# Optimization experiments

Hardware: AMD Instinct MI355X
Metric: run time of the kernel (lower is better)

## Reference

```python
import jax, jax.numpy as jnp
import numpy as np

TEMP = 1.0
EPS = 1e-3  # keras LayerNormalization default epsilon


def _ln(x, g, b):
    m = jnp.mean(x, -1, keepdims=True)
    v = jnp.mean((x - m) ** 2, -1, keepdims=True)
    return g * (x - m) * jax.lax.rsqrt(v + EPS) + b


def setup_inputs() -> dict:
    key = jax.random.key(0)
    ks = jax.random.split(key, 16)
    B, N, C, A, F = 8, 2048, 64, 256, 128
    r = lambda k, s: (jax.random.normal(ks[k], s) * 0.02).astype(jnp.float32)
    z = lambda n: jnp.zeros((n,), jnp.float32)
    return {
        'spatial': jax.random.normal(ks[0], (B, N, C), jnp.float32),
        'frequency': jax.random.normal(ks[1], (B, N, C), jnp.float32),
        'wavelet': jax.random.normal(ks[2], (B, N, C), jnp.float32),
        'Ws': r(3, (C, A)), 'bs': z(A),
        'Wf': r(4, (C, A)), 'bf': z(A),
        'Ww': r(5, (C, A)), 'bw': z(A),
        'g1': jnp.ones((A,), jnp.float32), 'b1': z(A),
        'Wk': r(6, (A, F)), 'bk': z(F),
        'Wq': r(7, (A, F)), 'bq': z(F),
        'Wt': r(8, (A, F)), 'bt': z(F),
        'Wg': r(9, (F + 3, F)), 'bg': z(F),
        'Wfu': r(10, (3 * F, F)), 'bfu': z(F),
        'Wdf': r(11, (F, F)), 'bdf': z(F),
        'g2': jnp.ones((F,), jnp.float32), 'b2': z(F),
    }


def _forward(spatial, frequency, wavelet, Ws, bs, Wf, bf, Ww, bw, g1, b1,
             Wk, bk, Wq, bq, Wt, bt, Wg, bg, Wfu, bfu, Wdf, bdf, g2, b2):
    B = spatial.shape[0]
    # FeatureAlignment: per-domain Dense + shared LayerNorm
    aligned = [
        _ln(spatial @ Ws + bs, g1, b1),
        _ln(frequency @ Wf + bf, g1, b1),
        _ln(wavelet @ Ww + bw, g1, b1),
    ]  # each [B, N, A]
    # DomainCorrelation
    K = [a @ Wk + bk for a in aligned]  # [B, N, F]
    Q = [a @ Wq + bq for a in aligned]
    corr = jnp.zeros((B, 3, 3), spatial.dtype)
    for i in range(3):
        for j in range(i, 3):
            # queries from domain j, keys from domain i (as in original)
            s = jax.nn.softmax(jnp.einsum('bnd,bmd->bnm', Q[j], K[i]) / TEMP, axis=-1)
            m = jnp.mean(s, axis=(1, 2))  # [B]
            corr = corr.at[:, i, j].set(m)
            if i != j:
                corr = corr.at[:, j, i].set(m)
    # NOTE: original applies softmax over the batch axis of the [B] row means
    dw = [jax.nn.softmax(jnp.mean(corr[:, i, :], axis=1)) for i in range(3)]  # each [B]
    # FeatureTransfer
    corr_mean = jnp.mean(corr, axis=1)  # [B, 3]
    enhanced = []
    for a, w in zip(aligned, dw):
        t = a @ Wt + bt  # [B, N, F]
        N = t.shape[1]
        gin = jnp.concatenate([t, jnp.broadcast_to(corr_mean[:, None, :], (B, N, 3))], axis=-1)
        gate = jax.nn.sigmoid(gin @ Wg + bg)
        enhanced.append(t * gate * w[:, None, None])
    fused = jnp.concatenate(enhanced, axis=-1) @ Wfu + bfu  # [B, N, F]
    out = _ln(fused @ Wdf + bdf, g2, b2)
    return out, corr, dw, enhanced


def reference(spatial, frequency, wavelet, Ws, bs, Wf, bf, Ww, bw, g1, b1,
              Wk, bk, Wq, bq, Wt, bt, Wg, bg, Wfu, bfu, Wdf, bdf, g2, b2):
    out, corr, dw, enh = _forward(spatial, frequency, wavelet, Ws, bs, Wf, bf, Ww, bw,
                                  g1, b1, Wk, bk, Wq, bq, Wt, bt, Wg, bg, Wfu, bfu,
                                  Wdf, bdf, g2, b2)
    return (out, corr, dw[0], dw[1], dw[2], enh[0], enh[1], enh[2])
```

## Files before the change

### kernel.cpp

```cpp
#include <hip/hip_runtime.h>
#include <math.h>


typedef __attribute__((ext_vector_type(8))) short short8;
typedef __attribute__((ext_vector_type(4))) float f32x4;
#define MFMA(a, b, c) __builtin_amdgcn_mfma_f32_16x16x32_bf16(a, b, c, 0, 0, 0)

#define NTOK 32

#define WD0_B 0u
#define WD1_B 32768u
#define WD2_B 65536u
#define WT_B  98304u
#define WG_B  163840u
#define WF0_B 196608u
#define WF1_B 229376u
#define WF2_B 262144u
#define WDF_B 294912u

__device__ __forceinline__ unsigned short bf16rtn(float v) {
    unsigned u = __float_as_uint(v);
    unsigned r = u + 0x7FFFu + ((u >> 16) & 1u);
    return (unsigned short)(r >> 16);
}
__device__ __forceinline__ void split2(float v, unsigned short& h, unsigned short& l) {
    h = bf16rtn(v);
    float hf = __uint_as_float(((unsigned)h) << 16);
    l = bf16rtn(v - hf);
}
__device__ __forceinline__ float bf2f(unsigned short h) {
    return __uint_as_float(((unsigned)h) << 16);
}

__global__ __launch_bounds__(256) void prep_kernel(
    const float* __restrict__ Ws, const float* __restrict__ Wf,
    const float* __restrict__ Ww, const float* __restrict__ Wt,
    const float* __restrict__ Wg, const float* __restrict__ Wfu,
    const float* __restrict__ Wdf, unsigned short* __restrict__ ws)
{
    int s = blockIdx.x * 256 + threadIdx.x;
    const float* src; int K, N; unsigned base, S; int fi;
    if (s < 2048)      { src = Ws;            K = 64;  N = 256; base = WD0_B; S = 16384; fi = s; }
    else if (s < 4096) { src = Wf;            K = 64;  N = 256; base = WD1_B; S = 16384; fi = s - 2048; }
    else if (s < 6144) { src = Ww;            K = 64;  N = 256; base = WD2_B; S = 16384; fi = s - 4096; }
    else if (s < 10240){ src = Wt;            K = 256; N = 128; base = WT_B;  S = 32768; fi = s - 6144; }
    else if (s < 12288){ src = Wg;            K = 128; N = 128; base = WG_B;  S = 16384; fi = s - 10240; }
    else if (s < 14336){ src = Wfu;           K = 128; N = 128; base = WF0_B; S = 16384; fi = s - 12288; }
    else if (s < 16384){ src = Wfu + 16384;   K = 128; N = 128; base = WF1_B; S = 16384; fi = s - 14336; }
    else if (s < 18432){ src = Wfu + 32768;   K = 128; N = 128; base = WF2_B; S = 16384; fi = s - 16384; }
    else               { src = Wdf;           K = 128; N = 128; base = WDF_B; S = 16384; fi = s - 18432; }
    const int lane = fi & 63, frag = fi >> 6;
    const int KC = K >> 5;
    const int nt = frag / KC, kc = frag - nt * KC;
    const int n  = nt * 16 + (lane & 15);
    const int k0 = kc * 32 + (lane >> 4) * 8;
    short8 hv, lv;
    #pragma unroll
    for (int j = 0; j < 8; ++j) {
        unsigned short h, l;
        split2(src[(k0 + j) * N + n], h, l);
        hv[j] = (short)h; lv[j] = (short)l;
    }
    *(short8*)&ws[base + (unsigned)fi * 8]     = hv;
    *(short8*)&ws[base + S + (unsigned)fi * 8] = lv;
}

__device__ __forceinline__ void gemm128(
    const unsigned short* __restrict__ wsB, unsigned S,
    const unsigned short* __restrict__ Ph, const unsigned short* __restrict__ Pl,
    int tokA, int quad, int wn, int lane, f32x4 acc[2])
{
    short8 Bh[2], Bl[2], Bh2[2], Bl2[2];
    #pragma unroll
    for (int i = 0; i < 2; ++i) {
        const unsigned short* bp = wsB + ((unsigned)((wn * 2 + i) * 4) * 64 + lane) * 8;
        Bh[i] = *(const short8*)bp; Bl[i] = *(const short8*)(bp + S);
    }
    #pragma unroll 1
    for (int kc = 0; kc < 4; ++kc) {
        if (kc < 3) {
            #pragma unroll
            for (int i = 0; i < 2; ++i) {
                const unsigned short* bp = wsB + ((unsigned)((wn * 2 + i) * 4 + kc + 1) * 64 + lane) * 8;
                Bh2[i] = *(const short8*)bp; Bl2[i] = *(const short8*)(bp + S);
            }
        }
        const int k = kc * 32 + quad * 8;
        const short8 Ah = *(const short8*)&Ph[tokA * 136 + k];
        const short8 Al = *(const short8*)&Pl[tokA * 136 + k];
        #pragma unroll
        for (int i = 0; i < 2; ++i) {
            acc[i] = MFMA(Ah, Bh[i], acc[i]);
            acc[i] = MFMA(Al, Bh[i], acc[i]);
            acc[i] = MFMA(Ah, Bl[i], acc[i]);
        }
        #pragma unroll
        for (int i = 0; i < 2; ++i) { Bh[i] = Bh2[i]; Bl[i] = Bl2[i]; }
    }
}

__global__ __launch_bounds__(512, 4) void mega_kernel(
    const float* __restrict__ x0, const float* __restrict__ x1,
    const float* __restrict__ x2,
    const float* __restrict__ bd0, const float* __restrict__ bd1,
    const float* __restrict__ bd2,
    const float* __restrict__ g1, const float* __restrict__ b1,
    const float* __restrict__ bt, const float* __restrict__ Wg,
    const float* __restrict__ bg, const float* __restrict__ bfu,
    const float* __restrict__ bdf, const float* __restrict__ g2,
    const float* __restrict__ b2,
    const unsigned short* __restrict__ ws,
    float* __restrict__ out, float* __restrict__ consts,
    float* __restrict__ e0, float* __restrict__ e1, float* __restrict__ e2)
{
    __shared__ __align__(16) unsigned char smem[52224];
    unsigned short* xh = (unsigned short*)smem;
    unsigned short* xl = xh + 32 * 72;
    unsigned short* th = (unsigned short*)smem;
    unsigned short* tl = th + 32 * 136;
    unsigned short* ah = (unsigned short*)(smem + 17408);
    unsigned short* al = ah + 32 * 264;
    float* ostage = (float*)(smem + 17408);
    float* psum   = (float*)(smem + 51200);

    const int tid = threadIdx.x, wave = tid >> 6, lane = tid & 63;
    const int lm = lane & 15, quad = lane >> 4;
    const int wn = wave & 3, wm = wave >> 2;
    const int row0 = blockIdx.x * NTOK;

    if (blockIdx.x == 0) {
        if (tid < 72) consts[tid] = 4.8828125e-4f;
        else if (tid < 96) consts[tid] = 0.125f;
    }

    int cA[4]; float g1c[4], b1c[4];
    #pragma unroll
    for (int i = 0; i < 4; ++i) { cA[i] = (wn * 4 + i) * 16 + lm; g1c[i] = g1[cA[i]]; b1c[i] = b1[cA[i]]; }
    int cT[2]; float btc[2], bgc[2], bdc[2], g2c[2], b2c[2];
    f32x4 facc[2];
    #pragma unroll
    for (int i = 0; i < 2; ++i) {
        const int c = (wn * 2 + i) * 16 + lm; cT[i] = c;
        btc[i] = bt[c];
        bgc[i] = bg[c] + 4.8828125e-4f * (Wg[16384 + c] + Wg[16512 + c] + Wg[16640 + c]);
        bdc[i] = bdf[c]; g2c[i] = g2[c]; b2c[i] = b2[c];
        const float bv = bfu[c];
        facc[i] = (f32x4){bv, bv, bv, bv};
    }

    const float* xs[3]  = {x0, x1, x2};
    const float* bds[3] = {bd0, bd1, bd2};
    float* es[3] = {e0, e1, e2};
    const unsigned WDB[3] = {WD0_B, WD1_B, WD2_B};
    const unsigned WFB[3] = {WF0_B, WF1_B, WF2_B};

    const int tokA = wm * 16 + lm;

    for (int d = 0; d < 3; ++d) {
        __syncthreads();
        {
            const int tok = tid >> 4, c4 = (tid & 15) * 4;
            const f32x4 v = __builtin_nontemporal_load(
                (const f32x4*)&xs[d][(row0 + tok) * 64 + c4]);
            unsigned short h0, l0, h1, l1, h2, l2, h3, l3;
            split2(v.x, h0, l0); split2(v.y, h1, l1);
            split2(v.z, h2, l2); split2(v.w, h3, l3);
            *(ushort4*)&xh[tok * 72 + c4] = make_ushort4(h0, h1, h2, h3);
            *(ushort4*)&xl[tok * 72 + c4] = make_ushort4(l0, l1, l2, l3);
        }
        __syncthreads();

        f32x4 acc[4];
        {
            const float* bdp = bds[d];
            #pragma unroll
            for (int i = 0; i < 4; ++i) { const float bv = bdp[cA[i]]; acc[i] = (f32x4){bv, bv, bv, bv}; }
        }
        #pragma unroll
        for (int kc = 0; kc < 2; ++kc) {
            const int k = kc * 32 + quad * 8;
            const short8 Ah = *(const short8*)&xh[tokA * 72 + k];
            const short8 Al = *(const short8*)&xl[tokA * 72 + k];
            #pragma unroll
            for (int i = 0; i < 4; ++i) {
                const unsigned short* bp = ws + WDB[d] + ((unsigned)((wn * 4 + i) * 2 + kc) * 64 + lane) * 8;
                const short8 Bh = *(const short8*)bp;
                const short8 Bl = *(const short8*)(bp + 16384);
                acc[i] = MFMA(Ah, Bh, acc[i]);
                acc[i] = MFMA(Al, Bh, acc[i]);
                acc[i] = MFMA(Ah, Bl, acc[i]);
            }
        }
        {
            float s[4], qq[4];
            #pragma unroll
            for (int r = 0; r < 4; ++r) {
                s[r] = 0.f; qq[r] = 0.f;
                #pragma unroll
                for (int i = 0; i < 4; ++i) { const float v = acc[i][r]; s[r] += v; qq[r] += v * v; }
            }
            #pragma unroll
            for (int off = 1; off < 16; off <<= 1) {
                #pragma unroll
                for (int r = 0; r < 4; ++r) { s[r] += __shfl_xor(s[r], off); qq[r] += __shfl_xor(qq[r], off); }
            }
            if (lm == 0) {
                #pragma unroll
                for (int r = 0; r < 4; ++r) {
                    const int row = wm * 16 + quad * 4 + r;
                    psum[row * 8 + wn * 2]     = s[r];
                    psum[row * 8 + wn * 2 + 1] = qq[r];
                }
            }
        }
        __syncthreads();
        #pragma unroll
        for (int r = 0; r < 4; ++r) {
            const int row = wm * 16 + quad * 4 + r;
            float S = 0.f, Q = 0.f;
            #pragma unroll
            for (int w = 0; w < 4; ++w) { S += psum[row * 8 + w * 2]; Q += psum[row * 8 + w * 2 + 1]; }
            const float m  = S * (1.f / 256.f);
            const float rs = rsqrtf(Q * (1.f / 256.f) - m * m + 1e-3f);
            #pragma unroll
            for (int i = 0; i < 4; ++i) {
                const float v = (acc[i][r] - m) * rs * g1c[i] + b1c[i];
                unsigned short h, l; split2(v, h, l);
                ah[row * 264 + cA[i]] = h; al[row * 264 + cA[i]] = l;
            }
        }
        __syncthreads();

        f32x4 tac[2];
        #pragma unroll
        for (int i = 0; i < 2; ++i) tac[i] = (f32x4){btc[i], btc[i], btc[i], btc[i]};
        {
            short8 Bh[2], Bl[2], Bh2[2], Bl2[2];
            #pragma unroll
            for (int i = 0; i < 2; ++i) {
                const unsigned short* bp = ws + WT_B + ((unsigned)((wn * 2 + i) * 8) * 64 + lane) * 8;
                Bh[i] = *(const short8*)bp; Bl[i] = *(const short8*)(bp + 32768);
            }
            #pragma unroll 1
            for (int kc = 0; kc < 8; ++kc) {
                if (kc < 7) {
                    #pragma unroll
                    for (int i = 0; i < 2; ++i) {
                        const unsigned short* bp = ws + WT_B + ((unsigned)((wn * 2 + i) * 8 + kc + 1) * 64 + lane) * 8;
                        Bh2[i] = *(const short8*)bp; Bl2[i] = *(const short8*)(bp + 32768);
                    }
                }
                const int k = kc * 32 + quad * 8;
                const short8 Ah = *(const short8*)&ah[tokA * 264 + k];
                const short8 Al = *(const short8*)&al[tokA * 264 + k];
                #pragma unroll
                for (int i = 0; i < 2; ++i) {
                    tac[i] = MFMA(Ah, Bh[i], tac[i]);
                    tac[i] = MFMA(Al, Bh[i], tac[i]);
                    tac[i] = MFMA(Ah, Bl[i], tac[i]);
                }
                #pragma unroll
                for (int i = 0; i < 2; ++i) { Bh[i] = Bh2[i]; Bl[i] = Bl2[i]; }
            }
        }
        __syncthreads();
        #pragma unroll
        for (int i = 0; i < 2; ++i)
            #pragma unroll
            for (int r = 0; r < 4; ++r) {
                const int row = wm * 16 + quad * 4 + r;
                unsigned short h, l; split2(tac[i][r], h, l);
                th[row * 136 + cT[i]] = h; tl[row * 136 + cT[i]] = l;
            }
        __syncthreads();

        f32x4 zac[2];
        #pragma unroll
        for (int i = 0; i < 2; ++i) zac[i] = (f32x4){bgc[i], bgc[i], bgc[i], bgc[i]};
        gemm128(ws + WG_B, 16384, th, tl, tokA, quad, wn, lane, zac);

        float er[2][4];
        #pragma unroll
        for (int i = 0; i < 2; ++i)
            #pragma unroll
            for (int r = 0; r < 4; ++r) {
                const int row = wm * 16 + quad * 4 + r;
                const float tv = bf2f(th[row * 136 + cT[i]]) + bf2f(tl[row * 136 + cT[i]]);
                er[i][r] = tv * (1.f / (1.f + __expf(-zac[i][r]))) * 0.125f;
            }
        __syncthreads();
        #pragma unroll
        for (int i = 0; i < 2; ++i)
            #pragma unroll
            for (int r = 0; r < 4; ++r) {
                const int row = wm * 16 + quad * 4 + r;
                unsigned short h, l; split2(er[i][r], h, l);
                th[row * 136 + cT[i]] = h; tl[row * 136 + cT[i]] = l;
            }
        __syncthreads();

        #pragma unroll
        for (int p = 0; p < 2; ++p) {
            const int row = (tid >> 5) + p * 16;
            const int c4 = (tid & 31) * 4;
            const ushort4 h0 = *(const ushort4*)&th[row * 136 + c4];
            const ushort4 l0 = *(const ushort4*)&tl[row * 136 + c4];
            f32x4 o = {bf2f(h0.x) + bf2f(l0.x), bf2f(h0.y) + bf2f(l0.y),
                       bf2f(h0.z) + bf2f(l0.z), bf2f(h0.w) + bf2f(l0.w)};
            __builtin_nontemporal_store(o, (f32x4*)(es[d] + (row0 + row) * 128 + c4));
        }

        gemm128(ws + WFB[d], 16384, th, tl, tokA, quad, wn, lane, facc);
    }

    __syncthreads();
    #pragma unroll
    for (int i = 0; i < 2; ++i)
        #pragma unroll
        for (int r = 0; r < 4; ++r) {
            const int row = wm * 16 + quad * 4 + r;
            unsigned short h, l; split2(facc[i][r], h, l);
            th[row * 136 + cT[i]] = h; tl[row * 136 + cT[i]] = l;
        }
    __syncthreads();

    f32x4 dac[2];
    #pragma unroll
    for (int i = 0; i < 2; ++i) dac[i] = (f32x4){bdc[i], bdc[i], bdc[i], bdc[i]};
    gemm128(ws + WDF_B, 16384, th, tl, tokA, quad, wn, lane, dac);

    {
        float s[4], qq[4];
        #pragma unroll
        for (int r = 0; r < 4; ++r) {
            s[r] = dac[0][r] + dac[1][r];
            qq[r] = dac[0][r] * dac[0][r] + dac[1][r] * dac[1][r];
        }
        #pragma unroll
        for (int off = 1; off < 16; off <<= 1) {
            #pragma unroll
            for (int r = 0; r < 4; ++r) { s[r] += __shfl_xor(s[r], off); qq[r] += __shfl_xor(qq[r], off); }
        }
        if (lm == 0) {
            #pragma unroll
            for (int r = 0; r < 4; ++r) {
                const int row = wm * 16 + quad * 4 + r;
                psum[row * 8 + wn * 2]     = s[r];
                psum[row * 8 + wn * 2 + 1] = qq[r];
            }
        }
    }
    __syncthreads();
    #pragma unroll
    for (int r = 0; r < 4; ++r) {
        const int row = wm * 16 + quad * 4 + r;
        float S = 0.f, Q = 0.f;
        #pragma unroll
        for (int w = 0; w < 4; ++w) { S += psum[row * 8 + w * 2]; Q += psum[row * 8 + w * 2 + 1]; }
        const float m  = S * (1.f / 128.f);
        const float rs = rsqrtf(Q * (1.f / 128.f) - m * m + 1e-3f);
        #pragma unroll
        for (int i = 0; i < 2; ++i)
            ostage[row * 128 + cT[i]] = (dac[i][r] - m) * rs * g2c[i] + b2c[i];
    }
    __syncthreads();
    #pragma unroll
    for (int p = 0; p < 2; ++p) {
        const int row = (tid >> 5) + p * 16;
        const int c4 = (tid & 31) * 4;
        const f32x4 o = *(const f32x4*)&ostage[row * 128 + c4];
        __builtin_nontemporal_store(o, (f32x4*)(out + (row0 + row) * 128 + c4));
    }
}

extern "C" void kernel_launch(void* const* d_in, const int* in_sizes, int n_in,
                              void* d_out, int out_size, void* d_ws, size_t ws_size,
                              hipStream_t stream) {
    const float* spatial   = (const float*)d_in[0];
    const float* frequency = (const float*)d_in[1];
    const float* wavelet   = (const float*)d_in[2];
    const float* Ws  = (const float*)d_in[3];
    const float* bs  = (const float*)d_in[4];
    const float* Wf  = (const float*)d_in[5];
    const float* bf  = (const float*)d_in[6];
    const float* Ww  = (const float*)d_in[7];
    const float* bw  = (const float*)d_in[8];
    const float* g1  = (const float*)d_in[9];
    const float* b1  = (const float*)d_in[10];
    const float* Wt  = (const float*)d_in[15];
    const float* bt  = (const float*)d_in[16];
    const float* Wg  = (const float*)d_in[17];
    const float* bg  = (const float*)d_in[18];
    const float* Wfu = (const float*)d_in[19];
    const float* bfu = (const float*)d_in[20];
    const float* Wdf = (const float*)d_in[21];
    const float* bdf = (const float*)d_in[22];
    const float* g2  = (const float*)d_in[23];
    const float* b2  = (const float*)d_in[24];

    float* out    = (float*)d_out;
    float* consts = out + 2097152;
    float* enh0   = out + 2097248;
    float* enh1   = out + 4194400;
    float* enh2   = out + 6291552;
    unsigned short* wsp = (unsigned short*)d_ws;

    prep_kernel<<<80, 256, 0, stream>>>(Ws, Wf, Ww, Wt, Wg, Wfu, Wdf, wsp);
    mega_kernel<<<16384 / NTOK, 512, 0, stream>>>(
        spatial, frequency, wavelet, bs, bf, bw, g1, b1,
        bt, Wg, bg, bfu, bdf, g2, b2, wsp,
        out, consts, enh0, enh1, enh2);
}
```

Measured before the change: 194.6 us.

## Retile waves to own column strips across all tokens, preloading full weight fragments

Each of the 8 waves now owns a 16- or 32-column strip over all 32 tokens, replacing the 2x4 token-by-column wave grid. Each B weight fragment is therefore loaded from global memory once and reused for two token tiles, and all K-chunk fragments are preloaded into registers before the MFMA loop. The layer-norm partial sums move to separate 8-wide S/Q arrays so they can be read as vectors. The t values are kept in registers so the gate step no longer re-reads them from shared memory. In exchange, register pressure rises under the 512-thread, 4-block launch bound.

```diff
diff --git a/kernel.cpp b/kernel.cpp
--- a/kernel.cpp
+++ b/kernel.cpp
@@ -65,40 +65,6 @@
     *(short8*)&ws[base + S + (unsigned)fi * 8] = lv;
 }
 
-__device__ __forceinline__ void gemm128(
-    const unsigned short* __restrict__ wsB, unsigned S,
-    const unsigned short* __restrict__ Ph, const unsigned short* __restrict__ Pl,
-    int tokA, int quad, int wn, int lane, f32x4 acc[2])
-{
-    short8 Bh[2], Bl[2], Bh2[2], Bl2[2];
-    #pragma unroll
-    for (int i = 0; i < 2; ++i) {
-        const unsigned short* bp = wsB + ((unsigned)((wn * 2 + i) * 4) * 64 + lane) * 8;
-        Bh[i] = *(const short8*)bp; Bl[i] = *(const short8*)(bp + S);
-    }
-    #pragma unroll 1
-    for (int kc = 0; kc < 4; ++kc) {
-        if (kc < 3) {
-            #pragma unroll
-            for (int i = 0; i < 2; ++i) {
-                const unsigned short* bp = wsB + ((unsigned)((wn * 2 + i) * 4 + kc + 1) * 64 + lane) * 8;
-                Bh2[i] = *(const short8*)bp; Bl2[i] = *(const short8*)(bp + S);
-            }
-        }
-        const int k = kc * 32 + quad * 8;
-        const short8 Ah = *(const short8*)&Ph[tokA * 136 + k];
-        const short8 Al = *(const short8*)&Pl[tokA * 136 + k];
-        #pragma unroll
-        for (int i = 0; i < 2; ++i) {
-            acc[i] = MFMA(Ah, Bh[i], acc[i]);
-            acc[i] = MFMA(Al, Bh[i], acc[i]);
-            acc[i] = MFMA(Ah, Bl[i], acc[i]);
-        }
-        #pragma unroll
-        for (int i = 0; i < 2; ++i) { Bh[i] = Bh2[i]; Bl[i] = Bl2[i]; }
-    }
-}
-
 __global__ __launch_bounds__(512, 4) void mega_kernel(
     const float* __restrict__ x0, const float* __restrict__ x1,
     const float* __restrict__ x2,
@@ -113,7 +79,7 @@
     float* __restrict__ out, float* __restrict__ consts,
     float* __restrict__ e0, float* __restrict__ e1, float* __restrict__ e2)
 {
-    __shared__ __align__(16) unsigned char smem[52224];
+    __shared__ __align__(16) unsigned char smem[53248];
     unsigned short* xh = (unsigned short*)smem;
     unsigned short* xl = xh + 32 * 72;
     unsigned short* th = (unsigned short*)smem;
@@ -121,40 +87,34 @@
     unsigned short* ah = (unsigned short*)(smem + 17408);
     unsigned short* al = ah + 32 * 264;
     float* ostage = (float*)(smem + 17408);
-    float* psum   = (float*)(smem + 51200);
-
-    const int tid = threadIdx.x, wave = tid >> 6, lane = tid & 63;
+    float* psumS  = (float*)(smem + 51200);
+    float* psumQ  = psumS + 32 * 8;
+
+    const int tid = threadIdx.x, wv = tid >> 6, lane = tid & 63;
     const int lm = lane & 15, quad = lane >> 4;
-    const int wn = wave & 3, wm = wave >> 2;
     const int row0 = blockIdx.x * NTOK;
+    const int tok0 = lm, tok1 = lm + 16;
 
     if (blockIdx.x == 0) {
         if (tid < 72) consts[tid] = 4.8828125e-4f;
         else if (tid < 96) consts[tid] = 0.125f;
     }
 
-    int cA[4]; float g1c[4], b1c[4];
-    #pragma unroll
-    for (int i = 0; i < 4; ++i) { cA[i] = (wn * 4 + i) * 16 + lm; g1c[i] = g1[cA[i]]; b1c[i] = b1[cA[i]]; }
-    int cT[2]; float btc[2], bgc[2], bdc[2], g2c[2], b2c[2];
+    int cA[2]; float g1c[2], b1c[2];
+    #pragma unroll
+    for (int i = 0; i < 2; ++i) { cA[i] = (wv * 2 + i) * 16 + lm; g1c[i] = g1[cA[i]]; b1c[i] = b1[cA[i]]; }
+    const int cT = wv * 16 + lm;
+    const float btc = bt[cT];
+    const float bgc = bg[cT] + 4.8828125e-4f * (Wg[16384 + cT] + Wg[16512 + cT] + Wg[16640 + cT]);
+    const float bdc = bdf[cT], g2c = g2[cT], b2c = b2[cT];
     f32x4 facc[2];
-    #pragma unroll
-    for (int i = 0; i < 2; ++i) {
-        const int c = (wn * 2 + i) * 16 + lm; cT[i] = c;
-        btc[i] = bt[c];
-        bgc[i] = bg[c] + 4.8828125e-4f * (Wg[16384 + c] + Wg[16512 + c] + Wg[16640 + c]);
-        bdc[i] = bdf[c]; g2c[i] = g2[c]; b2c[i] = b2[c];
-        const float bv = bfu[c];
-        facc[i] = (f32x4){bv, bv, bv, bv};
-    }
+    { const float bv = bfu[cT]; facc[0] = (f32x4){bv, bv, bv, bv}; facc[1] = facc[0]; }
 
     const float* xs[3]  = {x0, x1, x2};
     const float* bds[3] = {bd0, bd1, bd2};
     float* es[3] = {e0, e1, e2};
     const unsigned WDB[3] = {WD0_B, WD1_B, WD2_B};
     const unsigned WFB[3] = {WF0_B, WF1_B, WF2_B};
-
-    const int tokA = wm * 16 + lm;
 
     for (int d = 0; d < 3; ++d) {
         __syncthreads();
@@ -170,132 +130,164 @@
         }
         __syncthreads();
 
-        f32x4 acc[4];
+        f32x4 acc[2][2];
         {
             const float* bdp = bds[d];
             #pragma unroll
-            for (int i = 0; i < 4; ++i) { const float bv = bdp[cA[i]]; acc[i] = (f32x4){bv, bv, bv, bv}; }
-        }
-        #pragma unroll
-        for (int kc = 0; kc < 2; ++kc) {
-            const int k = kc * 32 + quad * 8;
-            const short8 Ah = *(const short8*)&xh[tokA * 72 + k];
-            const short8 Al = *(const short8*)&xl[tokA * 72 + k];
-            #pragma unroll
-            for (int i = 0; i < 4; ++i) {
-                const unsigned short* bp = ws + WDB[d] + ((unsigned)((wn * 4 + i) * 2 + kc) * 64 + lane) * 8;
-                const short8 Bh = *(const short8*)bp;
-                const short8 Bl = *(const short8*)(bp + 16384);
-                acc[i] = MFMA(Ah, Bh, acc[i]);
-                acc[i] = MFMA(Al, Bh, acc[i]);
-                acc[i] = MFMA(Ah, Bl, acc[i]);
-            }
-        }
-        {
-            float s[4], qq[4];
-            #pragma unroll
-            for (int r = 0; r < 4; ++r) {
-                s[r] = 0.f; qq[r] = 0.f;
+            for (int i = 0; i < 2; ++i) {
+                const float bv = bdp[cA[i]];
+                acc[i][0] = (f32x4){bv, bv, bv, bv}; acc[i][1] = acc[i][0];
+            }
+        }
+        {
+            short8 Bh[2][2], Bl[2][2];
+            #pragma unroll
+            for (int i = 0; i < 2; ++i)
                 #pragma unroll
-                for (int i = 0; i < 4; ++i) { const float v = acc[i][r]; s[r] += v; qq[r] += v * v; }
-            }
-            #pragma unroll
-            for (int off = 1; off < 16; off <<= 1) {
+                for (int kc = 0; kc < 2; ++kc) {
+                    const unsigned short* bp = ws + WDB[d] +
+                        ((unsigned)((wv * 2 + i) * 2 + kc) * 64 + lane) * 8;
+                    Bh[i][kc] = *(const short8*)bp;
+                    Bl[i][kc] = *(const short8*)(bp + 16384);
+                }
+            #pragma unroll
+            for (int kc = 0; kc < 2; ++kc) {
+                const int k = kc * 32 + quad * 8;
+                const short8 Ah0 = *(const short8*)&xh[tok0 * 72 + k];
+                const short8 Al0 = *(const short8*)&xl[tok0 * 72 + k];
+                const short8 Ah1 = *(const short8*)&xh[tok1 * 72 + k];
+                const short8 Al1 = *(const short8*)&xl[tok1 * 72 + k];
                 #pragma unroll
-                for (int r = 0; r < 4; ++r) { s[r] += __shfl_xor(s[r], off); qq[r] += __shfl_xor(qq[r], off); }
-            }
-            if (lm == 0) {
+                for (int i = 0; i < 2; ++i) {
+                    acc[i][0] = MFMA(Ah0, Bh[i][kc], acc[i][0]);
+                    acc[i][0] = MFMA(Al0, Bh[i][kc], acc[i][0]);
+                    acc[i][0] = MFMA(Ah0, Bl[i][kc], acc[i][0]);
+                    acc[i][1] = MFMA(Ah1, Bh[i][kc], acc[i][1]);
+                    acc[i][1] = MFMA(Al1, Bh[i][kc], acc[i][1]);
+                    acc[i][1] = MFMA(Ah1, Bl[i][kc], acc[i][1]);
+                }
+            }
+        }
+        {
+            #pragma unroll
+            for (int m = 0; m < 2; ++m)
                 #pragma unroll
                 for (int r = 0; r < 4; ++r) {
-                    const int row = wm * 16 + quad * 4 + r;
-                    psum[row * 8 + wn * 2]     = s[r];
-                    psum[row * 8 + wn * 2 + 1] = qq[r];
-                }
-            }
-        }
-        __syncthreads();
-        #pragma unroll
-        for (int r = 0; r < 4; ++r) {
-            const int row = wm * 16 + quad * 4 + r;
-            float S = 0.f, Q = 0.f;
-            #pragma unroll
-            for (int w = 0; w < 4; ++w) { S += psum[row * 8 + w * 2]; Q += psum[row * 8 + w * 2 + 1]; }
-            const float m  = S * (1.f / 256.f);
-            const float rs = rsqrtf(Q * (1.f / 256.f) - m * m + 1e-3f);
-            #pragma unroll
-            for (int i = 0; i < 4; ++i) {
-                const float v = (acc[i][r] - m) * rs * g1c[i] + b1c[i];
-                unsigned short h, l; split2(v, h, l);
-                ah[row * 264 + cA[i]] = h; al[row * 264 + cA[i]] = l;
-            }
-        }
-        __syncthreads();
-
-        f32x4 tac[2];
-        #pragma unroll
-        for (int i = 0; i < 2; ++i) tac[i] = (f32x4){btc[i], btc[i], btc[i], btc[i]};
-        {
-            short8 Bh[2], Bl[2], Bh2[2], Bl2[2];
-            #pragma unroll
-            for (int i = 0; i < 2; ++i) {
-                const unsigned short* bp = ws + WT_B + ((unsigned)((wn * 2 + i) * 8) * 64 + lane) * 8;
-                Bh[i] = *(const short8*)bp; Bl[i] = *(const short8*)(bp + 32768);
-            }
-            #pragma unroll 1
-            for (int kc = 0; kc < 8; ++kc) {
-                if (kc < 7) {
+                    float s = acc[0][m][r] + acc[1][m][r];
+                    float q = acc[0][m][r] * acc[0][m][r] + acc[1][m][r] * acc[1][m][r];
                     #pragma unroll
-                    for (int i = 0; i < 2; ++i) {
-                        const unsigned short* bp = ws + WT_B + ((unsigned)((wn * 2 + i) * 8 + kc + 1) * 64 + lane) * 8;
-                        Bh2[i] = *(const short8*)bp; Bl2[i] = *(const short8*)(bp + 32768);
+                    for (int off = 1; off < 16; off <<= 1) {
+                        s += __shfl_xor(s, off); q += __shfl_xor(q, off);
+                    }
+                    if (lm == 0) {
+                        const int row = m * 16 + quad * 4 + r;
+                        psumS[row * 8 + wv] = s;
+                        psumQ[row * 8 + wv] = q;
                     }
                 }
-                const int k = kc * 32 + quad * 8;
-                const short8 Ah = *(const short8*)&ah[tokA * 264 + k];
-                const short8 Al = *(const short8*)&al[tokA * 264 + k];
+        }
+        __syncthreads();
+        #pragma unroll
+        for (int m = 0; m < 2; ++m)
+            #pragma unroll
+            for (int r = 0; r < 4; ++r) {
+                const int row = m * 16 + quad * 4 + r;
+                const float4 s0 = *(const float4*)&psumS[row * 8];
+                const float4 s1 = *(const float4*)&psumS[row * 8 + 4];
+                const float4 q0 = *(const float4*)&psumQ[row * 8];
+                const float4 q1 = *(const float4*)&psumQ[row * 8 + 4];
+                const float S = s0.x + s0.y + s0.z + s0.w + s1.x + s1.y + s1.z + s1.w;
+                const float Q = q0.x + q0.y + q0.z + q0.w + q1.x + q1.y + q1.z + q1.w;
+                const float mean = S * (1.f / 256.f);
+                const float rs = rsqrtf(Q * (1.f / 256.f) - mean * mean + 1e-3f);
                 #pragma unroll
                 for (int i = 0; i < 2; ++i) {
-                    tac[i] = MFMA(Ah, Bh[i], tac[i]);
-                    tac[i] = MFMA(Al, Bh[i], tac[i]);
-                    tac[i] = MFMA(Ah, Bl[i], tac[i]);
+                    const float v = (acc[i][m][r] - mean) * rs * g1c[i] + b1c[i];
+                    unsigned short h, l; split2(v, h, l);
+                    ah[row * 264 + cA[i]] = h; al[row * 264 + cA[i]] = l;
                 }
-                #pragma unroll
-                for (int i = 0; i < 2; ++i) { Bh[i] = Bh2[i]; Bl[i] = Bl2[i]; }
-            }
-        }
-        __syncthreads();
-        #pragma unroll
-        for (int i = 0; i < 2; ++i)
+            }
+        __syncthreads();
+
+        f32x4 tac[2];
+        tac[0] = (f32x4){btc, btc, btc, btc}; tac[1] = tac[0];
+        {
+            short8 Bh[8], Bl[8];
+            #pragma unroll
+            for (int kc = 0; kc < 8; ++kc) {
+                const unsigned short* bp = ws + WT_B + ((unsigned)(wv * 8 + kc) * 64 + lane) * 8;
+                Bh[kc] = *(const short8*)bp;
+                Bl[kc] = *(const short8*)(bp + 32768);
+            }
+            #pragma unroll
+            for (int kc = 0; kc < 8; ++kc) {
+                const int k = kc * 32 + quad * 8;
+                const short8 Ah0 = *(const short8*)&ah[tok0 * 264 + k];
+                const short8 Al0 = *(const short8*)&al[tok0 * 264 + k];
+                const short8 Ah1 = *(const short8*)&ah[tok1 * 264 + k];
+                const short8 Al1 = *(const short8*)&al[tok1 * 264 + k];
+                tac[0] = MFMA(Ah0, Bh[kc], tac[0]);
+                tac[0] = MFMA(Al0, Bh[kc], tac[0]);
+                tac[0] = MFMA(Ah0, Bl[kc], tac[0]);
+                tac[1] = MFMA(Ah1, Bh[kc], tac[1]);
+                tac[1] = MFMA(Al1, Bh[kc], tac[1]);
+                tac[1] = MFMA(Ah1, Bl[kc], tac[1]);
+            }
+        }
+        __syncthreads();
+        unsigned short tsp[2][4][2];
+        #pragma unroll
+        for (int m = 0; m < 2; ++m)
             #pragma unroll
             for (int r = 0; r < 4; ++r) {
-                const int row = wm * 16 + quad * 4 + r;
-                unsigned short h, l; split2(tac[i][r], h, l);
-                th[row * 136 + cT[i]] = h; tl[row * 136 + cT[i]] = l;
+                const int row = m * 16 + quad * 4 + r;
+                unsigned short h, l; split2(tac[m][r], h, l);
+                tsp[m][r][0] = h; tsp[m][r][1] = l;
+                th[row * 136 + cT] = h; tl[row * 136 + cT] = l;
             }
         __syncthreads();
 
         f32x4 zac[2];
-        #pragma unroll
-        for (int i = 0; i < 2; ++i) zac[i] = (f32x4){bgc[i], bgc[i], bgc[i], bgc[i]};
-        gemm128(ws + WG_B, 16384, th, tl, tokA, quad, wn, lane, zac);
-
+        zac[0] = (f32x4){bgc, bgc, bgc, bgc}; zac[1] = zac[0];
+        {
+            short8 Bh[4], Bl[4];
+            #pragma unroll
+            for (int kc = 0; kc < 4; ++kc) {
+                const unsigned short* bp = ws + WG_B + ((unsigned)(wv * 4 + kc) * 64 + lane) * 8;
+                Bh[kc] = *(const short8*)bp;
+                Bl[kc] = *(const short8*)(bp + 16384);
+            }
+            #pragma unroll
+            for (int kc = 0; kc < 4; ++kc) {
+                const int k = kc * 32 + quad * 8;
+                const short8 Ah0 = *(const short8*)&th[tok0 * 136 + k];
+                const short8 Al0 = *(const short8*)&tl[tok0 * 136 + k];
+                const short8 Ah1 = *(const short8*)&th[tok1 * 136 + k];
+                const short8 Al1 = *(const short8*)&tl[tok1 * 136 + k];
+                zac[0] = MFMA(Ah0, Bh[kc], zac[0]);
+                zac[0] = MFMA(Al0, Bh[kc], zac[0]);
+                zac[0] = MFMA(Ah0, Bl[kc], zac[0]);
+                zac[1] = MFMA(Ah1, Bh[kc], zac[1]);
+                zac[1] = MFMA(Al1, Bh[kc], zac[1]);
+                zac[1] = MFMA(Ah1, Bl[kc], zac[1]);
+            }
+        }
         float er[2][4];
         #pragma unroll
-        for (int i = 0; i < 2; ++i)
+        for (int m = 0; m < 2; ++m)
             #pragma unroll
             for (int r = 0; r < 4; ++r) {
-                const int row = wm * 16 + quad * 4 + r;
-                const float tv = bf2f(th[row * 136 + cT[i]]) + bf2f(tl[row * 136 + cT[i]]);
-                er[i][r] = tv * (1.f / (1.f + __expf(-zac[i][r]))) * 0.125f;
-            }
-        __syncthreads();
-        #pragma unroll
-        for (int i = 0; i < 2; ++i)
+                const float tv = bf2f(tsp[m][r][0]) + bf2f(tsp[m][r][1]);
+                er[m][r] = tv * (1.f / (1.f + __expf(-zac[m][r]))) * 0.125f;
+            }
+        __syncthreads();
+        #pragma unroll
+        for (int m = 0; m < 2; ++m)
             #pragma unroll
             for (int r = 0; r < 4; ++r) {
-                const int row = wm * 16 + quad * 4 + r;
-                unsigned short h, l; split2(er[i][r], h, l);
-                th[row * 136 + cT[i]] = h; tl[row * 136 + cT[i]] = l;
+                const int row = m * 16 + quad * 4 + r;
+                unsigned short h, l; split2(er[m][r], h, l);
+                th[row * 136 + cT] = h; tl[row * 136 + cT] = l;
             }
         __syncthreads();
 
@@ -310,59 +302,100 @@
             __builtin_nontemporal_store(o, (f32x4*)(es[d] + (row0 + row) * 128 + c4));
         }
 
-        gemm128(ws + WFB[d], 16384, th, tl, tokA, quad, wn, lane, facc);
+        {
+            short8 Bh[4], Bl[4];
+            #pragma unroll
+            for (int kc = 0; kc < 4; ++kc) {
+                const unsigned short* bp = ws + WFB[d] + ((unsigned)(wv * 4 + kc) * 64 + lane) * 8;
+                Bh[kc] = *(const short8*)bp;
+                Bl[kc] = *(const short8*)(bp + 16384);
+            }
+            #pragma unroll
+            for (int kc = 0; kc < 4; ++kc) {
+                const int k = kc * 32 + quad * 8;
+                const short8 Ah0 = *(const short8*)&th[tok0 * 136 + k];
+                const short8 Al0 = *(const short8*)&tl[tok0 * 136 + k];
+                const short8 Ah1 = *(const short8*)&th[tok1 * 136 + k];
+                const short8 Al1 = *(const short8*)&tl[tok1 * 136 + k];
+                facc[0] = MFMA(Ah0, Bh[kc], facc[0]);
+                facc[0] = MFMA(Al0, Bh[kc], facc[0]);
+                facc[0] = MFMA(Ah0, Bl[kc], facc[0]);
+                facc[1] = MFMA(Ah1, Bh[kc], facc[1]);
+                facc[1] = MFMA(Al1, Bh[kc], facc[1]);
+                facc[1] = MFMA(Ah1, Bl[kc], facc[1]);
+            }
+        }
     }
 
     __syncthreads();
     #pragma unroll
-    for (int i = 0; i < 2; ++i)
+    for (int m = 0; m < 2; ++m)
         #pragma unroll
         for (int r = 0; r < 4; ++r) {
-            const int row = wm * 16 + quad * 4 + r;
-            unsigned short h, l; split2(facc[i][r], h, l);
-            th[row * 136 + cT[i]] = h; tl[row * 136 + cT[i]] = l;
+            const int row = m * 16 + quad * 4 + r;
+            unsigned short h, l; split2(facc[m][r], h, l);
+            th[row * 136 + cT] = h; tl[row * 136 + cT] = l;
         }
     __syncthreads();
 
     f32x4 dac[2];
-    #pragma unroll
-    for (int i = 0; i < 2; ++i) dac[i] = (f32x4){bdc[i], bdc[i], bdc[i], bdc[i]};
-    gemm128(ws + WDF_B, 16384, th, tl, tokA, quad, wn, lane, dac);
-
+    dac[0] = (f32x4){bdc, bdc, bdc, bdc}; dac[1] = dac[0];
     {
-        float s[4], qq[4];
+        short8 Bh[4], Bl[4];
+        #pragma unroll
+        for (int kc = 0; kc < 4; ++kc) {
+            const unsigned short* bp = ws + WDF_B + ((unsigned)(wv * 4 + kc) * 64 + lane) * 8;
+            Bh[kc] = *(const short8*)bp;
+            Bl[kc] = *(const short8*)(bp + 16384);
+        }
+        #pragma unroll
+        for (int kc = 0; kc < 4; ++kc) {
+            const int k = kc * 32 + quad * 8;
+            const short8 Ah0 = *(const short8*)&th[tok0 * 136 + k];
+            const short8 Al0 = *(const short8*)&tl[tok0 * 136 + k];
+            const short8 Ah1 = *(const short8*)&th[tok1 * 136 + k];
+            const short8 Al1 = *(const short8*)&tl[tok1 * 136 + k];
+            dac[0] = MFMA(Ah0, Bh[kc], dac[0]);
+            dac[0] = MFMA(Al0, Bh[kc], dac[0]);
+            dac[0] = MFMA(Ah0, Bl[kc], dac[0]);
+            dac[1] = MFMA(Ah1, Bh[kc], dac[1]);
+            dac[1] = MFMA(Al1, Bh[kc], dac[1]);
+            dac[1] = MFMA(Ah1, Bl[kc], dac[1]);
+        }
+    }
+
+    #pragma unroll
+    for (int m = 0; m < 2; ++m)
         #pragma unroll
         for (int r = 0; r < 4; ++r) {
-            s[r] = dac[0][r] + dac[1][r];
-            qq[r] = dac[0][r] * dac[0][r] + dac[1][r] * dac[1][r];
-        }
-        #pragma unroll
-        for (int off = 1; off < 16; off <<= 1) {
-            #pragma unroll
-            for (int r = 0; r < 4; ++r) { s[r] += __shfl_xor(s[r], off); qq[r] += __shfl_xor(qq[r], off); }
-        }
-        if (lm == 0) {
-            #pragma unroll
-            for (int r = 0; r < 4; ++r) {
-                const int row = wm * 16 + quad * 4 + r;
-                psum[row * 8 + wn * 2]     = s[r];
-                psum[row * 8 + wn * 2 + 1] = qq[r];
-            }
-        }
-    }
+            float s = dac[m][r];
+            float q = dac[m][r] * dac[m][r];
+            #pragma unroll
+            for (int off = 1; off < 16; off <<= 1) {
+                s += __shfl_xor(s, off); q += __shfl_xor(q, off);
+            }
+            if (lm == 0) {
+                const int row = m * 16 + quad * 4 + r;
+                psumS[row * 8 + wv] = s;
+                psumQ[row * 8 + wv] = q;
+            }
+        }
     __syncthreads();
     #pragma unroll
-    for (int r = 0; r < 4; ++r) {
-        const int row = wm * 16 + quad * 4 + r;
-        float S = 0.f, Q = 0.f;
-        #pragma unroll
-        for (int w = 0; w < 4; ++w) { S += psum[row * 8 + w * 2]; Q += psum[row * 8 + w * 2 + 1]; }
-        const float m  = S * (1.f / 128.f);
-        const float rs = rsqrtf(Q * (1.f / 128.f) - m * m + 1e-3f);
-        #pragma unroll
-        for (int i = 0; i < 2; ++i)
-            ostage[row * 128 + cT[i]] = (dac[i][r] - m) * rs * g2c[i] + b2c[i];
-    }
+    for (int m = 0; m < 2; ++m)
+        #pragma unroll
+        for (int r = 0; r < 4; ++r) {
+            const int row = m * 16 + quad * 4 + r;
+            const float4 s0 = *(const float4*)&psumS[row * 8];
+            const float4 s1 = *(const float4*)&psumS[row * 8 + 4];
+            const float4 q0 = *(const float4*)&psumQ[row * 8];
+            const float4 q1 = *(const float4*)&psumQ[row * 8 + 4];
+            const float S = s0.x + s0.y + s0.z + s0.w + s1.x + s1.y + s1.z + s1.w;
+            const float Q = q0.x + q0.y + q0.z + q0.w + q1.x + q1.y + q1.z + q1.w;
+            const float mean = S * (1.f / 128.f);
+            const float rs = rsqrtf(Q * (1.f / 128.f) - mean * mean + 1e-3f);
+            ostage[row * 128 + cT] = (dac[m][r] - mean) * rs * g2c + b2c;
+        }
     __syncthreads();
     #pragma unroll
     for (int p = 0; p < 2; ++p) {
```

Measured after the change: 204.8 us. +5.2%, slower.
